# Performance work log

Hardware: AMD Instinct MI355X
Metric: run time of the kernel (lower is better)

Reference implementation:

```python
import jax, jax.numpy as jnp
import numpy as np

N_SUPPORT = 32768
N_QUERY = 16384
D = 512
K = 32
U = 128
NEG_BIG = -1e30  # masked-out attention logit; all-masked class -> uniform weights == mean fallback


def setup_inputs() -> dict:
    key = jax.random.key(0)
    k1, k2, k3, k4, k5 = jax.random.split(key, 5)
    query = jax.random.normal(k1, (N_QUERY, D), dtype=jnp.float32)
    support = jax.random.normal(k2, (N_SUPPORT, D), dtype=jnp.float32)
    labels = jax.random.randint(k3, (N_SUPPORT,), 0, K, dtype=jnp.int32)
    # Xavier-normal-ish init for per-class projection V (U,D) and attention vector w (U,1)
    V = jax.random.normal(k4, (K, U, D), dtype=jnp.float32) * np.float32(np.sqrt(2.0 / (U + D)))
    w = jax.random.normal(k5, (K, U), dtype=jnp.float32) * np.float32(np.sqrt(2.0 / (U + 1)))
    return {"query_embeddings": query, "support_embeddings": support,
            "support_labels": labels, "V": V, "w": w}


def reference(query_embeddings, support_embeddings, support_labels, V, w):
    # --- attention-weighted prototypes (vectorized over classes via masked softmax) ---
    # projected[k,n,u] = tanh(V[k] @ x_n)
    projected = jnp.tanh(jnp.einsum('nd,kud->knu', support_embeddings, V))
    attn_logits = jnp.einsum('knu,ku->kn', projected, w)              # (K, N)
    mask = support_labels[None, :] == jnp.arange(K, dtype=support_labels.dtype)[:, None]
    attn_logits = jnp.where(mask, attn_logits, NEG_BIG)
    # per-class softmax over support samples; an empty class yields uniform weights,
    # i.e. prototype = mean(embeddings) -- exactly the torch fallback branch.
    attn = jax.nn.softmax(attn_logits, axis=1)                        # (K, N)
    prototypes = jnp.einsum('kn,nd->kd', attn, support_embeddings)    # (K, D)

    # --- squared-euclidean distance classification ---
    q2 = jnp.sum(query_embeddings * query_embeddings, axis=1, keepdims=True)   # (B, 1)
    p2 = jnp.sum(prototypes * prototypes, axis=1)[None, :]                     # (1, K)
    dists = q2 + p2 - 2.0 * (query_embeddings @ prototypes.T)                  # (B, K)
    return jax.nn.log_softmax(-dists, axis=1)
```

## Files before the change

kernel.cpp:

```cpp
#include <hip/hip_runtime.h>
#include <hip/hip_bf16.h>

#define N_SUPPORT 32768
#define N_QUERY   16384
#define DIM       512
#define NCLS      32
#define NU        128
#define NBLK      (N_SUPPORT / 256)

#define OFF_IDX      0
#define OFF_COUNT    131072
#define OFF_START    131200
#define OFF_M        131456
#define OFF_Z        131584
#define OFF_P2       131712
#define OFF_LOGIT    132096
#define OFF_PRAW     263168
#define OFF_PROTO    328704
#define OFF_BHIST    394240
#define OFF_BOFFS    410624
#define OFF_VBF      458752
#define OFF_PBF      4653056
#define OFF_INV      4718592
#define OFF_XS       4849664

typedef __attribute__((ext_vector_type(8))) short short8;
typedef __attribute__((ext_vector_type(4))) short short4v;
typedef __attribute__((ext_vector_type(4))) float f32x4;

typedef __attribute__((address_space(3))) unsigned int lds_u32;
typedef const __attribute__((address_space(1))) unsigned int glb_u32;

__device__ inline unsigned short f2bf(float f) {
    unsigned int x = __builtin_bit_cast(unsigned int, f);
    unsigned int r = x + 0x7fffu + ((x >> 16) & 1u);
    return (unsigned short)(r >> 16);
}
__device__ inline float bf2f(unsigned short h) {
    unsigned int u = ((unsigned int)h) << 16;
    return __builtin_bit_cast(float, u);
}

__device__ inline short8 pack_bf8(float4 f0, float4 f1) {
    short8 pk;
    pk[0] = f2bf(f0.x); pk[1] = f2bf(f0.y); pk[2] = f2bf(f0.z); pk[3] = f2bf(f0.w);
    pk[4] = f2bf(f1.x); pk[5] = f2bf(f1.y); pk[6] = f2bf(f1.z); pk[7] = f2bf(f1.w);
    return pk;
}

__device__ inline void pack_hilo(float4 f0, float4 f1, short8& hi, short8& lo) {
    float v[8] = {f0.x, f0.y, f0.z, f0.w, f1.x, f1.y, f1.z, f1.w};
    #pragma unroll
    for (int i = 0; i < 8; i++) {
        unsigned short h = f2bf(v[i]);
        hi[i] = (short)h;
        lo[i] = (short)f2bf(v[i] - bf2f(h));
    }
}

__global__ void k_vcast(const float* __restrict__ V, short* __restrict__ Vbf,
                        float* __restrict__ praw, const int* __restrict__ labels,
                        int* __restrict__ bhist) {
    __shared__ int h[NCLS];
    int tid = threadIdx.x;
    bool dohist = (blockIdx.x < NBLK);
    if (dohist) {
        if (tid < NCLS) h[tid] = 0;
        __syncthreads();
        atomicAdd(&h[labels[blockIdx.x * 256 + tid]], 1);
    }
    int i = blockIdx.x * 256 + tid;
    int ob = i * 4;
    int j0  = ob & 7;
    int s   = (ob >> 3) & 7;
    int u   = (ob >> 6) & 127;
    int c   = (ob >> 13) & 7;
    int k   = ob >> 16;
    int d   = c * 64 + ((s ^ (u & 7)) * 8) + j0;
    float4 f = *(const float4*)(V + ((size_t)(k * 128 + u) * DIM + d));
    short4v o;
    o[0] = f2bf(f.x); o[1] = f2bf(f.y); o[2] = f2bf(f.z); o[3] = f2bf(f.w);
    *(short4v*)(Vbf + (size_t)ob) = o;
    if (i < (NCLS * DIM) / 4) *(float4*)(praw + i * 4) = make_float4(0.f, 0.f, 0.f, 0.f);
    if (dohist) {
        __syncthreads();
        if (tid < NCLS) bhist[blockIdx.x * NCLS + tid] = h[tid];
    }
}

__global__ void k_scan2(const int* __restrict__ bhist, int* __restrict__ boffs,
                        int* __restrict__ start, int* __restrict__ count) {
    __shared__ int tot[NCLS];
    int tid = threadIdx.x;
    if (tid < NCLS) {
        int s = 0;
        for (int b = 0; b < NBLK; b++) {
            boffs[b * NCLS + tid] = s;
            s += bhist[b * NCLS + tid];
        }
        tot[tid] = s;
    }
    __syncthreads();
    if (tid == 0) {
        int run = 0;
        for (int k = 0; k < NCLS; k++) {
            start[k] = run;
            count[k] = tot[k];
            run += tot[k];
        }
        start[NCLS] = run;
    }
}

__global__ void k_scatter(const int* __restrict__ labels, const int* __restrict__ boffs,
                          const int* __restrict__ start, int* __restrict__ idx_c,
                          int* __restrict__ inv) {
    __shared__ int whist[4][NCLS];
    int tid = threadIdx.x;
    int n = blockIdx.x * 256 + tid;
    int l = labels[n];
    int lane = tid & 63, wid = tid >> 6;
    unsigned long long mymask = 0ull;
    #pragma unroll
    for (int k = 0; k < NCLS; k++) {
        unsigned long long mk = __ballot(l == k);
        if (k == l) mymask = mk;
        if (lane == k) whist[wid][k] = __popcll(mk);
    }
    int rank = __popcll(mymask & ((1ull << lane) - 1ull));
    __syncthreads();
    int wbase = 0;
    for (int w = 0; w < wid; w++) wbase += whist[w][l];
    int pos = start[l] + boffs[blockIdx.x * NCLS + l] + wbase + rank;
    idx_c[pos] = n;
    inv[n] = (pos << 3) | ((pos - start[l]) & 7);
}

__launch_bounds__(256, 1)
__global__ void k_gather(const float* __restrict__ support, const int* __restrict__ inv,
                         short* __restrict__ xs) {
    int t = threadIdx.x;
    int l = t & 63, wv = t >> 6;
    int rowbase = blockIdx.x * 64;
    #pragma unroll 4
    for (int i = 0; i < 16; i++) {
        int n = rowbase + wv + 4 * i;
        const float* src = support + (size_t)n * DIM + l * 8;
        float4 f0 = *(const float4*)src;
        float4 f1 = *(const float4*)(src + 4);
        int iv = inv[n];
        int pos = iv >> 3, swz = iv & 7;
        *(short8*)&xs[(size_t)pos * 512 + ((l ^ swz) * 8)] = pack_bf8(f0, f1);
    }
}

__launch_bounds__(256, 1)
__global__ void k_logits(const short* __restrict__ xs, const short* __restrict__ Vbf,
                         const float* __restrict__ w,
                         const int* __restrict__ start, const int* __restrict__ count,
                         float* __restrict__ logit_c) {
    int k = blockIdx.y;
    int cnt = count[k];
    int base = blockIdx.x * 32;
    if (base >= cnt) return;
    int M = min(32, cnt - base);
    int s0 = start[k] + base;
    int t = threadIdx.x;

    __shared__ __align__(16) short Xs[32 * 512];
    __shared__ float part[4][32];

    int l = t & 63, wv = t >> 6;
    int lo16 = l & 15, hi4 = l >> 4;

    const short* xsrc = xs + (size_t)s0 * 512;
    #pragma unroll
    for (int rep = 0; rep < 8; rep++) {
        int u = t + 256 * rep;
        __builtin_amdgcn_global_load_lds((glb_u32*)(xsrc + (size_t)u * 8),
                                         (lds_u32*)&Xs[u * 8], 16, 0, 0);
    }

    const short* Vk = Vbf + (size_t)k * (8 * 128 * 64);
    short8 vreg[4][2][2];
    #pragma unroll
    for (int c = 0; c < 4; c++)
        #pragma unroll
        for (int ks = 0; ks < 2; ks++)
            #pragma unroll
            for (int nt = 0; nt < 2; nt++) {
                int u = wv * 32 + nt * 16 + lo16;
                int q = ks * 4 + hi4;
                vreg[c][ks][nt] = *(const short8*)(Vk + (size_t)c * 8192 + (size_t)u * 64 + ((q ^ (u & 7)) * 8));
            }

    f32x4 acc[2][2];
    #pragma unroll
    for (int mt = 0; mt < 2; mt++)
        #pragma unroll
        for (int nt = 0; nt < 2; nt++) acc[mt][nt] = (f32x4){0.f, 0.f, 0.f, 0.f};

    __syncthreads();

#define COMPUTE(c, vb) { _Pragma("unroll")                                        \
    for (int ks = 0; ks < 2; ks++) {                                              \
        short8 a[2];                                                              \
        _Pragma("unroll")                                                         \
        for (int mt = 0; mt < 2; mt++) {                                          \
            int ar = mt * 16 + lo16;                                              \
            int cu = (c) * 8 + ks * 4 + hi4;                                      \
            a[mt] = *(short8*)&Xs[ar * 512 + ((cu ^ (ar & 7)) * 8)];              \
        }                                                                         \
        _Pragma("unroll")                                                         \
        for (int mt = 0; mt < 2; mt++)                                            \
            _Pragma("unroll")                                                     \
            for (int nt = 0; nt < 2; nt++)                                        \
                acc[mt][nt] = __builtin_amdgcn_mfma_f32_16x16x32_bf16(a[mt], vb[ks][nt], acc[mt][nt], 0, 0, 0); \
    } }

    #pragma unroll
    for (int c = 0; c < 4; c++) COMPUTE(c, vreg[c]);

    #pragma unroll
    for (int c = 0; c < 4; c++)
        #pragma unroll
        for (int ks = 0; ks < 2; ks++)
            #pragma unroll
            for (int nt = 0; nt < 2; nt++) {
                int u = wv * 32 + nt * 16 + lo16;
                int q = ks * 4 + hi4;
                vreg[c][ks][nt] = *(const short8*)(Vk + (size_t)(c + 4) * 8192 + (size_t)u * 64 + ((q ^ (u & 7)) * 8));
            }
    #pragma unroll
    for (int c = 0; c < 4; c++) COMPUTE(c + 4, vreg[c]);
#undef COMPUTE

    float w0 = w[k * NU + wv * 32 + lo16];
    float w1 = w[k * NU + wv * 32 + 16 + lo16];
    #pragma unroll
    for (int mt = 0; mt < 2; mt++) {
        #pragma unroll
        for (int r = 0; r < 4; r++) {
            float val = tanhf(acc[mt][0][r]) * w0 + tanhf(acc[mt][1][r]) * w1;
            val += __shfl_xor(val, 1);
            val += __shfl_xor(val, 2);
            val += __shfl_xor(val, 4);
            val += __shfl_xor(val, 8);
            if (lo16 == 0) part[wv][mt * 16 + hi4 * 4 + r] = val;
        }
    }
    __syncthreads();
    if (t < M) {
        logit_c[s0 + t] = part[0][t] + part[1][t] + part[2][t] + part[3][t];
    }
}

__global__ void k_mz(const float* __restrict__ logit_c, const int* __restrict__ start,
                     const int* __restrict__ count, float* __restrict__ m, float* __restrict__ Z) {
    int k = blockIdx.x;
    int cnt = count[k], s0 = start[k];
    int tid = threadIdx.x;
    __shared__ float red[256];
    float mx = -1e30f;
    for (int i = tid; i < cnt; i += 256) mx = fmaxf(mx, logit_c[s0 + i]);
    red[tid] = mx; __syncthreads();
    for (int off = 128; off > 0; off >>= 1) {
        if (tid < off) red[tid] = fmaxf(red[tid], red[tid + off]);
        __syncthreads();
    }
    float mk = red[0];
    __syncthreads();
    float s = 0.f;
    for (int i = tid; i < cnt; i += 256) s += expf(logit_c[s0 + i] - mk);
    red[tid] = s; __syncthreads();
    for (int off = 128; off > 0; off >>= 1) {
        if (tid < off) red[tid] += red[tid + off];
        __syncthreads();
    }
    if (tid == 0) { m[k] = mk; Z[k] = red[0]; }
}

__launch_bounds__(512, 1)
__global__ void k_proto(const float* __restrict__ support, const int* __restrict__ idx_c,
                        const float* __restrict__ logit_c, const int* __restrict__ start,
                        const int* __restrict__ count, const float* __restrict__ m,
                        float* __restrict__ praw) {
    int k = blockIdx.y;
    int cnt = count[k];
    int base = blockIdx.x * 64;
    if (base >= cnt) return;
    int M = min(64, cnt - base);
    int s0 = start[k] + base;
    __shared__ float wts[64];
    __shared__ int sid[64];
    int t = threadIdx.x;
    if (t < 64) {
        sid[t] = idx_c[s0 + ((t < M) ? t : 0)];
        wts[t] = (t < M) ? expf(logit_c[s0 + t] - m[k]) : 0.f;
    }
    __syncthreads();
    int d = t;
    float a = 0.f;
    for (int s = 0; s < 64; s += 4) {
        float r0 = support[(size_t)sid[s + 0] * DIM + d];
        float r1 = support[(size_t)sid[s + 1] * DIM + d];
        float r2 = support[(size_t)sid[s + 2] * DIM + d];
        float r3 = support[(size_t)sid[s + 3] * DIM + d];
        a += wts[s] * r0 + wts[s + 1] * r1 + wts[s + 2] * r2 + wts[s + 3] * r3;
    }
    atomicAdd(&praw[k * DIM + d], a);
}

__global__ void k_protonorm(const float* __restrict__ support, const float* __restrict__ praw,
                            const float* __restrict__ Z, const int* __restrict__ count,
                            float* __restrict__ proto, float* __restrict__ p2,
                            short* __restrict__ Pbf) {
    int k = blockIdx.x;
    int tid = threadIdx.x;
    int cnt = count[k];
    __shared__ float red[256];
    float pv[2];
    if (cnt > 0) {
        float inv = 1.f / Z[k];
        #pragma unroll
        for (int i = 0; i < 2; i++) pv[i] = praw[k * DIM + tid + i * 256] * inv;
    } else {
        #pragma unroll
        for (int i = 0; i < 2; i++) {
            int d = tid + i * 256;
            float s = 0.f;
            for (int n = 0; n < N_SUPPORT; n++) s += support[(size_t)n * DIM + d];
            pv[i] = s * (1.f / N_SUPPORT);
        }
    }
    float acc = 0.f;
    #pragma unroll
    for (int i = 0; i < 2; i++) {
        int d = tid + i * 256;
        proto[k * DIM + d] = pv[i];
        acc += pv[i] * pv[i];
        int c = d >> 6, off = d & 63, o = off >> 3, j = off & 7;
        int s = o ^ (k & 7);
        int pos = (c * 32 + k) * 64 + s * 8 + j;
        unsigned short hi = f2bf(pv[i]);
        Pbf[pos] = (short)hi;
        Pbf[NCLS * DIM + pos] = (short)f2bf(pv[i] - bf2f(hi));
    }
    red[tid] = acc; __syncthreads();
    for (int off = 128; off > 0; off >>= 1) {
        if (tid < off) red[tid] += red[tid + off];
        __syncthreads();
    }
    if (tid == 0) p2[k] = red[0];
}

__launch_bounds__(256, 1)
__global__ void k_dist(const float* __restrict__ query, const short* __restrict__ Pbf,
                       const float* __restrict__ p2, float* __restrict__ out) {
    __shared__ __align__(16) short Ph[NCLS * DIM];
    __shared__ __align__(16) short Pl[NCLS * DIM];
    __shared__ __align__(16) short Qh[2][64 * 64];
    __shared__ __align__(16) short Ql[2][64 * 64];
    int t = threadIdx.x;
    int qbase = blockIdx.x * 64;
    int l = t & 63, wv = t >> 6;
    int lo16 = l & 15, hi4 = l >> 4;

    #pragma unroll
    for (int rep = 0; rep < 8; rep++) {
        int u = t + 256 * rep;
        ((short8*)Ph)[u] = ((const short8*)Pbf)[u];
        ((short8*)Pl)[u] = ((const short8*)(Pbf + NCLS * DIM))[u];
    }

    int qrow[2], qslot[2], qdst[2];
    const float* qsrc[2];
    #pragma unroll
    for (int rep = 0; rep < 2; rep++) {
        int u = t + 256 * rep;
        qrow[rep] = u >> 3; qslot[rep] = u & 7;
        qdst[rep] = qrow[rep] * 64 + ((qslot[rep] ^ (qrow[rep] & 7)) * 8);
        qsrc[rep] = query + (size_t)(qbase + qrow[rep]) * DIM + qslot[rep] * 8;
    }

    f32x4 acc[2];
    acc[0] = (f32x4){0.f, 0.f, 0.f, 0.f};
    acc[1] = (f32x4){0.f, 0.f, 0.f, 0.f};

    float4 qa[2][2], qb[2][2];
#define LOADQ(d, c) { _Pragma("unroll") for (int rep = 0; rep < 2; rep++) { \
        d[rep][0] = *(const float4*)(qsrc[rep] + (c) * 64);                 \
        d[rep][1] = *(const float4*)(qsrc[rep] + (c) * 64 + 4); } }
#define WRITEQ(buf, d) { _Pragma("unroll") for (int rep = 0; rep < 2; rep++) { \
        short8 hi8, lo8;                                                        \
        pack_hilo(d[rep][0], d[rep][1], hi8, lo8);                              \
        *(short8*)&Qh[buf][qdst[rep]] = hi8;                                    \
        *(short8*)&Ql[buf][qdst[rep]] = lo8; } }

    LOADQ(qa, 0);
    LOADQ(qb, 1);
    WRITEQ(0, qa);

    for (int c = 0; c < 8; ++c) {
        int cur = c & 1;
        __syncthreads();
        if (c + 2 < 8) {
            if (cur == 0) { LOADQ(qa, c + 2); }
            else          { LOADQ(qb, c + 2); }
        }
        #pragma unroll
        for (int ks = 0; ks < 2; ks++) {
            int arow = wv * 16 + lo16;
            int asw = ((ks * 4 + hi4) ^ (arow & 7)) * 8;
            short8 ah = *(short8*)&Qh[cur][arow * 64 + asw];
            short8 al = *(short8*)&Ql[cur][arow * 64 + asw];
            #pragma unroll
            for (int nt = 0; nt < 2; nt++) {
                int brow = nt * 16 + lo16;
                int pos = (c * 32 + brow) * 64 + (((ks * 4 + hi4) ^ (brow & 7)) * 8);
                short8 bh = *(short8*)&Ph[pos];
                short8 bl = *(short8*)&Pl[pos];
                acc[nt] = __builtin_amdgcn_mfma_f32_16x16x32_bf16(ah, bh, acc[nt], 0, 0, 0);
                acc[nt] = __builtin_amdgcn_mfma_f32_16x16x32_bf16(ah, bl, acc[nt], 0, 0, 0);
                acc[nt] = __builtin_amdgcn_mfma_f32_16x16x32_bf16(al, bh, acc[nt], 0, 0, 0);
            }
        }
        if (c < 7) {
            if (cur == 0) { WRITEQ(1, qb); }
            else          { WRITEQ(0, qa); }
        }
    }
#undef LOADQ
#undef WRITEQ

    float p2v0 = p2[lo16];
    float p2v1 = p2[16 + lo16];
    #pragma unroll
    for (int r = 0; r < 4; r++) {
        float l0 = 2.f * acc[0][r] - p2v0;
        float l1 = 2.f * acc[1][r] - p2v1;
        float mx = fmaxf(l0, l1);
        mx = fmaxf(mx, __shfl_xor(mx, 1));
        mx = fmaxf(mx, __shfl_xor(mx, 2));
        mx = fmaxf(mx, __shfl_xor(mx, 4));
        mx = fmaxf(mx, __shfl_xor(mx, 8));
        float s = expf(l0 - mx) + expf(l1 - mx);
        s += __shfl_xor(s, 1);
        s += __shfl_xor(s, 2);
        s += __shfl_xor(s, 4);
        s += __shfl_xor(s, 8);
        float lse = mx + logf(s);
        int q = qbase + wv * 16 + hi4 * 4 + r;
        out[(size_t)q * NCLS + lo16] = l0 - lse;
        out[(size_t)q * NCLS + 16 + lo16] = l1 - lse;
    }
}

extern "C" void kernel_launch(void* const* d_in, const int* in_sizes, int n_in,
                              void* d_out, int out_size, void* d_ws, size_t ws_size,
                              hipStream_t stream) {
    const float* query   = (const float*)d_in[0];
    const float* support = (const float*)d_in[1];
    const int*   labels  = (const int*)d_in[2];
    const float* V       = (const float*)d_in[3];
    const float* w       = (const float*)d_in[4];
    float* out = (float*)d_out;
    char* ws = (char*)d_ws;

    int*   idx_c   = (int*)(ws + OFF_IDX);
    int*   count   = (int*)(ws + OFF_COUNT);
    int*   start   = (int*)(ws + OFF_START);
    float* m       = (float*)(ws + OFF_M);
    float* Z       = (float*)(ws + OFF_Z);
    float* p2      = (float*)(ws + OFF_P2);
    float* logit_c = (float*)(ws + OFF_LOGIT);
    float* praw    = (float*)(ws + OFF_PRAW);
    float* proto   = (float*)(ws + OFF_PROTO);
    int*   bhist   = (int*)(ws + OFF_BHIST);
    int*   boffs   = (int*)(ws + OFF_BOFFS);
    short* vbf     = (short*)(ws + OFF_VBF);
    short* pbf     = (short*)(ws + OFF_PBF);
    int*   inv     = (int*)(ws + OFF_INV);
    short* xsorted = (short*)(ws + OFF_XS);

    hipLaunchKernelGGL(k_vcast, dim3((NCLS * NU * DIM) / 1024), dim3(256), 0, stream,
                       V, vbf, praw, labels, bhist);
    hipLaunchKernelGGL(k_scan2, dim3(1), dim3(64), 0, stream, bhist, boffs, start, count);
    hipLaunchKernelGGL(k_scatter, dim3(NBLK), dim3(256), 0, stream, labels, boffs, start, idx_c, inv);
    hipLaunchKernelGGL(k_gather, dim3(N_SUPPORT / 64), dim3(256), 0, stream, support, inv, xsorted);
    hipLaunchKernelGGL(k_logits, dim3(64, NCLS), dim3(256), 0, stream,
                       xsorted, vbf, w, start, count, logit_c);
    hipLaunchKernelGGL(k_mz, dim3(NCLS), dim3(256), 0, stream, logit_c, start, count, m, Z);
    hipLaunchKernelGGL(k_proto, dim3(32, NCLS), dim3(512), 0, stream,
                       support, idx_c, logit_c, start, count, m, praw);
    hipLaunchKernelGGL(k_protonorm, dim3(NCLS), dim3(256), 0, stream,
                       support, praw, Z, count, proto, p2, pbf);
    hipLaunchKernelGGL(k_dist, dim3(N_QUERY / 64), dim3(256), 0, stream, query, pbf, p2, out);
}
```

Baseline: 83.58 us.

## Make k_logits persistent over four tiles with double-buffered LDS prefetch

Each k_logits block now handles four 32-row tiles of a class instead of one. It loads all eight V chunks into registers once and reuses them across the tiles. Support rows stream into two LDS buffers with async global_load_lds, and the next tile is prefetched while the current one is computed. This cuts repeated V loads and hides X-load latency, at the cost of four times fewer blocks (512 versus 2048), more registers for V, and explicit vmcnt/barrier synchronisation.

```diff
diff --git a/kernel.cpp b/kernel.cpp
--- a/kernel.cpp
+++ b/kernel.cpp
@@ -161,30 +161,20 @@
                          float* __restrict__ logit_c) {
     int k = blockIdx.y;
     int cnt = count[k];
-    int base = blockIdx.x * 32;
-    if (base >= cnt) return;
-    int M = min(32, cnt - base);
-    int s0 = start[k] + base;
+    int tb = blockIdx.x;
+    int s0k = start[k];
     int t = threadIdx.x;
 
-    __shared__ __align__(16) short Xs[32 * 512];
+    __shared__ __align__(16) short Xb[2][32 * 512];
     __shared__ float part[4][32];
 
     int l = t & 63, wv = t >> 6;
     int lo16 = l & 15, hi4 = l >> 4;
 
-    const short* xsrc = xs + (size_t)s0 * 512;
-    #pragma unroll
-    for (int rep = 0; rep < 8; rep++) {
-        int u = t + 256 * rep;
-        __builtin_amdgcn_global_load_lds((glb_u32*)(xsrc + (size_t)u * 8),
-                                         (lds_u32*)&Xs[u * 8], 16, 0, 0);
-    }
-
     const short* Vk = Vbf + (size_t)k * (8 * 128 * 64);
-    short8 vreg[4][2][2];
-    #pragma unroll
-    for (int c = 0; c < 4; c++)
+    short8 vreg[8][2][2];
+    #pragma unroll
+    for (int c = 0; c < 8; c++)
         #pragma unroll
         for (int ks = 0; ks < 2; ks++)
             #pragma unroll
@@ -194,65 +184,75 @@
                 vreg[c][ks][nt] = *(const short8*)(Vk + (size_t)c * 8192 + (size_t)u * 64 + ((q ^ (u & 7)) * 8));
             }
 
-    f32x4 acc[2][2];
-    #pragma unroll
-    for (int mt = 0; mt < 2; mt++)
-        #pragma unroll
-        for (int nt = 0; nt < 2; nt++) acc[mt][nt] = (f32x4){0.f, 0.f, 0.f, 0.f};
-
-    __syncthreads();
-
-#define COMPUTE(c, vb) { _Pragma("unroll")                                        \
-    for (int ks = 0; ks < 2; ks++) {                                              \
-        short8 a[2];                                                              \
-        _Pragma("unroll")                                                         \
-        for (int mt = 0; mt < 2; mt++) {                                          \
-            int ar = mt * 16 + lo16;                                              \
-            int cu = (c) * 8 + ks * 4 + hi4;                                      \
-            a[mt] = *(short8*)&Xs[ar * 512 + ((cu ^ (ar & 7)) * 8)];              \
-        }                                                                         \
-        _Pragma("unroll")                                                         \
-        for (int mt = 0; mt < 2; mt++)                                            \
-            _Pragma("unroll")                                                     \
-            for (int nt = 0; nt < 2; nt++)                                        \
-                acc[mt][nt] = __builtin_amdgcn_mfma_f32_16x16x32_bf16(a[mt], vb[ks][nt], acc[mt][nt], 0, 0, 0); \
-    } }
-
-    #pragma unroll
-    for (int c = 0; c < 4; c++) COMPUTE(c, vreg[c]);
-
-    #pragma unroll
-    for (int c = 0; c < 4; c++)
-        #pragma unroll
-        for (int ks = 0; ks < 2; ks++)
-            #pragma unroll
-            for (int nt = 0; nt < 2; nt++) {
-                int u = wv * 32 + nt * 16 + lo16;
-                int q = ks * 4 + hi4;
-                vreg[c][ks][nt] = *(const short8*)(Vk + (size_t)(c + 4) * 8192 + (size_t)u * 64 + ((q ^ (u & 7)) * 8));
-            }
-    #pragma unroll
-    for (int c = 0; c < 4; c++) COMPUTE(c + 4, vreg[c]);
-#undef COMPUTE
-
     float w0 = w[k * NU + wv * 32 + lo16];
     float w1 = w[k * NU + wv * 32 + 16 + lo16];
-    #pragma unroll
-    for (int mt = 0; mt < 2; mt++) {
-        #pragma unroll
-        for (int r = 0; r < 4; r++) {
-            float val = tanhf(acc[mt][0][r]) * w0 + tanhf(acc[mt][1][r]) * w1;
-            val += __shfl_xor(val, 1);
-            val += __shfl_xor(val, 2);
-            val += __shfl_xor(val, 4);
-            val += __shfl_xor(val, 8);
-            if (lo16 == 0) part[wv][mt * 16 + hi4 * 4 + r] = val;
-        }
-    }
-    __syncthreads();
-    if (t < M) {
-        logit_c[s0 + t] = part[0][t] + part[1][t] + part[2][t] + part[3][t];
-    }
+
+#define ISSUE(tt, buf) { int base_ = (tb * 4 + (tt)) * 32;                         \
+        int cb_ = (base_ < cnt) ? base_ : 0;                                       \
+        const short* src_ = xs + (size_t)(s0k + cb_) * 512;                        \
+        _Pragma("unroll") for (int rep = 0; rep < 8; rep++) {                      \
+            int u_ = t + 256 * rep;                                                \
+            __builtin_amdgcn_global_load_lds((glb_u32*)(src_ + (size_t)u_ * 8),    \
+                                             (lds_u32*)&Xb[buf][u_ * 8], 16, 0, 0);\
+        } }
+
+    ISSUE(0, 0);
+    ISSUE(1, 1);
+
+    #pragma unroll
+    for (int tt = 0; tt < 4; tt++) {
+        int cur = tt & 1;
+        if (tt < 3) { asm volatile("s_waitcnt vmcnt(8)" ::: "memory"); }
+        else        { asm volatile("s_waitcnt vmcnt(0)" ::: "memory"); }
+        __builtin_amdgcn_s_barrier();
+
+        int base = (tb * 4 + tt) * 32;
+        bool active = (base < cnt);
+        if (active) {
+            f32x4 acc[2][2];
+            #pragma unroll
+            for (int mt = 0; mt < 2; mt++)
+                #pragma unroll
+                for (int nt = 0; nt < 2; nt++) acc[mt][nt] = (f32x4){0.f, 0.f, 0.f, 0.f};
+            #pragma unroll
+            for (int c = 0; c < 8; c++)
+                #pragma unroll
+                for (int ks = 0; ks < 2; ks++) {
+                    short8 a[2];
+                    #pragma unroll
+                    for (int mt = 0; mt < 2; mt++) {
+                        int ar = mt * 16 + lo16;
+                        int cu = c * 8 + ks * 4 + hi4;
+                        a[mt] = *(short8*)&Xb[cur][ar * 512 + ((cu ^ (ar & 7)) * 8)];
+                    }
+                    #pragma unroll
+                    for (int mt = 0; mt < 2; mt++)
+                        #pragma unroll
+                        for (int nt = 0; nt < 2; nt++)
+                            acc[mt][nt] = __builtin_amdgcn_mfma_f32_16x16x32_bf16(a[mt], vreg[c][ks][nt], acc[mt][nt], 0, 0, 0);
+                }
+            #pragma unroll
+            for (int mt = 0; mt < 2; mt++) {
+                #pragma unroll
+                for (int r = 0; r < 4; r++) {
+                    float val = tanhf(acc[mt][0][r]) * w0 + tanhf(acc[mt][1][r]) * w1;
+                    val += __shfl_xor(val, 1);
+                    val += __shfl_xor(val, 2);
+                    val += __shfl_xor(val, 4);
+                    val += __shfl_xor(val, 8);
+                    if (lo16 == 0) part[wv][mt * 16 + hi4 * 4 + r] = val;
+                }
+            }
+        }
+        __builtin_amdgcn_s_barrier();
+        if (active && t < 32) {
+            int M = min(32, cnt - base);
+            if (t < M)
+                logit_c[s0k + base + t] = part[0][t] + part[1][t] + part[2][t] + part[3][t];
+        }
+        if (tt + 2 < 4) ISSUE(tt + 2, cur);
+    }
+#undef ISSUE
 }
 
 __global__ void k_mz(const float* __restrict__ logit_c, const int* __restrict__ start,
@@ -488,7 +488,7 @@
     hipLaunchKernelGGL(k_scan2, dim3(1), dim3(64), 0, stream, bhist, boffs, start, count);
     hipLaunchKernelGGL(k_scatter, dim3(NBLK), dim3(256), 0, stream, labels, boffs, start, idx_c, inv);
     hipLaunchKernelGGL(k_gather, dim3(N_SUPPORT / 64), dim3(256), 0, stream, support, inv, xsorted);
-    hipLaunchKernelGGL(k_logits, dim3(64, NCLS), dim3(256), 0, stream,
+    hipLaunchKernelGGL(k_logits, dim3(16, NCLS), dim3(256), 0, stream,
                        xsorted, vbf, w, start, count, logit_c);
     hipLaunchKernelGGL(k_mz, dim3(NCLS), dim3(256), 0, stream, logit_c, start, count, m, Z);
     hipLaunchKernelGGL(k_proto, dim3(32, NCLS), dim3(512), 0, stream,
```

Result: slower. 87.73 us (+5.0%).
